# Optimization experiments

Hardware: AMD Instinct MI355X
Metric: run time of the kernel (lower is better)

## Reference

```python
import jax, jax.numpy as jnp
import numpy as np

# --- config (mirrors EV_TGN init + data attributes) ---
WIDTH, HEIGHT, TIME_WINDOW = 640, 480, 1_000_000  # data.width/height/time_window
RADIUS_NORM = 0.01                                # args.radius
MAX_NEIGHBORS = 16                                # args.max_neighbors
WINDOW = 256                                      # backward candidate window (approximates per-pixel queues, max_queue_size=128)
B, NPG = 4, 32768                                 # num_graphs, events per graph
N = B * NPG
RADIUS_PX = int(RADIUS_NORM * WIDTH + 1)          # init_graph_creator
DELTA_T = int(RADIUS_NORM * TIME_WINDOW)


def setup_inputs() -> dict:
    key = jax.random.key(0)
    kxy, kt = jax.random.split(key)
    xy = jax.random.uniform(kxy, (N, 2), dtype=jnp.float32)
    # timestamps sorted within each graph (events arrive time-ordered)
    t = jnp.sort(jax.random.uniform(kt, (B, NPG), dtype=jnp.float32), axis=1).reshape(N, 1)
    pos = jnp.concatenate([xy, t], axis=1)  # normalized (x, y, t) in [0,1]
    batch = jnp.repeat(jnp.arange(B, dtype=jnp.int32), NPG)
    return {"pos": pos, "batch": batch}


def _build_edges(pos, batch):
    # denormalize_pos: (denorm * pos + 0.001).int()
    denorm = jnp.array([WIDTH, HEIGHT, TIME_WINDOW], dtype=jnp.float32)
    p = (denorm[None, :] * pos + 0.001).astype(jnp.int32)  # [N,3] int pixel/us coords

    n = p.shape[0]
    i_idx = jnp.arange(n, dtype=jnp.int32)[:, None]       # [N,1] destination
    off = jnp.arange(1, WINDOW + 1, dtype=jnp.int32)[None, :]  # [1,W] recency offsets
    j_idx = i_idx - off                                   # [N,W] candidate sources (most recent first)
    in_range = j_idx >= 0
    j_c = jnp.clip(j_idx, 0, n - 1)

    same_b = batch[j_c] == batch[:, None]
    dxy = p[:, None, :2] - p[j_c, :2]                     # [N,W,2]
    dist2 = jnp.sum(dxy * dxy, axis=-1)
    dt = p[:, None, 2] - p[j_c, 2]
    mask = in_range & same_b & (dist2 <= RADIUS_PX * RADIUS_PX) & (dt >= 0) & (dt <= DELTA_T)

    # keep the MAX_NEIGHBORS most recent valid neighbors per destination
    rank = jnp.cumsum(mask.astype(jnp.int32), axis=1)     # 1-based recency rank
    keep = mask & (rank <= MAX_NEIGHBORS)
    slot = jnp.where(keep, rank - 1, MAX_NEIGHBORS)       # dropped entries -> dummy column
    src = jnp.full((n, MAX_NEIGHBORS + 1), -1, dtype=jnp.int32)
    rows = jnp.broadcast_to(jnp.arange(n)[:, None], slot.shape)
    src = src.at[rows, slot].set(jnp.where(keep, j_idx, -1).astype(jnp.int32))
    src = src[:, :MAX_NEIGHBORS]                          # [N,K], -1 padded
    dst = jnp.broadcast_to(jnp.arange(n, dtype=jnp.int32)[:, None], src.shape)
    dst = jnp.where(src >= 0, dst, -1)
    # edge_index: row0 = source (earlier event), row1 = destination; -1 marks padding
    return jnp.stack([src.reshape(-1), dst.reshape(-1)], axis=0)


def reference(pos, batch):
    return _build_edges(pos, batch)
```

## Files before the change

kernel.cpp:

```cpp
#include <hip/hip_runtime.h>

#define NPG    32768
#define NTOT   131072
#define MAXN   16
#define RAD2   49
#define DTMAX  10000u
#define NPB    64
#define GX     20
#define GY     16
#define NCELL  (GX*GY)
#define SLOTS  16

__global__ __launch_bounds__(256, 5)
void tgn_edges_kernel(const float* __restrict__ pos, int* __restrict__ out) {
    __shared__ int2 sp[320];
    __shared__ int  cellcnt[NCELL];
    __shared__ int  cells[NCELL][SLOTS];
    __shared__ int  fin[NPB][MAXN];

    const int tid = threadIdx.x;
    const int b0  = blockIdx.x * NPB;

    {
        const int4 m1 = make_int4(-1, -1, -1, -1);
        int4* c4 = reinterpret_cast<int4*>(&cells[0][0]);
        #pragma unroll
        for (int k = 0; k < 5; ++k) c4[k * 256 + tid] = m1;
        cellcnt[tid] = 0;
        if (tid < NCELL - 256) cellcnt[256 + tid] = 0;
        reinterpret_cast<int4*>(&fin[0][0])[tid] = m1;
    }
    __syncthreads();

    #pragma unroll
    for (int s = 0; s < 2; ++s) {
        const int idx = s * 256 + tid;
        if (s == 0 || tid < 320 - 256) {
            const int node = b0 - 256 + idx;
            if (node >= 0) {
                const float x  = pos[3 * node + 0];
                const float y  = pos[3 * node + 1];
                const float tt = pos[3 * node + 2];
                const int px = (int)(__fadd_rn(__fmul_rn(640.0f,     x),  0.001f));
                const int py = (int)(__fadd_rn(__fmul_rn(480.0f,     y),  0.001f));
                const int pt = (int)(__fadd_rn(__fmul_rn(1000000.0f, tt), 0.001f));
                sp[idx] = make_int2(px | (py << 16), pt);
                const int cell = ((py * 2185) >> 16) * GX + (px >> 5);
                const int slot = atomicAdd(&cellcnt[cell], 1);
                if (slot < SLOTS) cells[cell][slot] = idx;
            }
        }
    }
    __syncthreads();

    const int n    = tid >> 2;
    const int qq   = tid & 3;
    const int lane = tid & 63;
    const int2 pown = sp[256 + n];
    const int x  = pown.x & 0xffff;
    const int y  = pown.x >> 16;
    const int it = pown.y;

    const int xlo = x > 7 ? x - 7 : 0;
    const int xhi = x < 632 ? x + 7 : 639;
    const int ylo = y > 7 ? y - 7 : 0;
    const int yhi = y < 472 ? y + 7 : 479;
    const int cx0 = xlo >> 5,              cx1 = xhi >> 5;
    const int cy0 = (ylo * 2185) >> 16,    cy1 = (yhi * 2185) >> 16;
    const int cx  = (qq & 1) ? cx1 : cx0;
    const int cy  = (qq & 2) ? cy1 : cy0;
    const bool dup = (((qq & 1) != 0) & (cx1 == cx0)) | (((qq & 2) != 0) & (cy1 == cy0));
    const int cell = cy * GX + cx;
    int c = dup ? 0 : cellcnt[cell];
    c = c > SLOTS ? SLOTS : c;

    const int boff   = b0 & (NPG - 1);
    const int idxmin = (256 - boff) > n ? (256 - boff) : n;
    const int idxmax = n + 255;

    unsigned bm = 0;
    if (c > 0) {
        const int4 s4 = *reinterpret_cast<const int4*>(&cells[cell][0]);
        const int sl[4] = {s4.x, s4.y, s4.z, s4.w};
        #pragma unroll
        for (int k = 0; k < 4; ++k) {
            const int idx = sl[k];
            bool ok = (k < c) & (idx >= idxmin) & (idx <= idxmax);
            const int ii = ok ? idx : 0;
            const int2 pj = sp[ii];
            const int dx = x - (pj.x & 0xffff);
            const int dy = y - (pj.x >> 16);
            const unsigned dt = (unsigned)(it - pj.y);
            ok = ok & (dx * dx + dy * dy <= RAD2) & (dt <= DTMAX);
            bm |= ok ? (1u << k) : 0u;
        }
        if (c > 4) {
            for (int k = 4; k < c; ++k) {
                const int idx = cells[cell][k];
                bool ok = (idx >= idxmin) & (idx <= idxmax);
                const int ii = ok ? idx : 0;
                const int2 pj = sp[ii];
                const int dx = x - (pj.x & 0xffff);
                const int dy = y - (pj.x >> 16);
                const unsigned dt = (unsigned)(it - pj.y);
                ok = ok & (dx * dx + dy * dy <= RAD2) & (dt <= DTMAX);
                bm |= ok ? (1u << k) : 0u;
            }
        }
    }

    const int gb = lane & ~3;
    unsigned bmq[4];
    int      clq[4];
    #pragma unroll
    for (int q2 = 0; q2 < 4; ++q2) {
        bmq[q2] = __shfl(bm,   gb + q2);
        clq[q2] = __shfl(cell, gb + q2);
    }
    if (qq == 0 && (bmq[0] | bmq[1] | bmq[2] | bmq[3])) {
        int m = 0;
        #pragma unroll
        for (int q2 = 0; q2 < 4; ++q2) {
            unsigned mm = bmq[q2];
            const int cl = clq[q2];
            while (mm) {
                const int k = __ffs(mm) - 1;
                mm &= mm - 1;
                const int j = b0 - 256 + cells[cl][k];
                int p = m < MAXN ? m : MAXN;
                while (p > 0 && fin[n][p - 1] < j) {
                    if (p < MAXN) fin[n][p] = fin[n][p - 1];
                    --p;
                }
                if (p < MAXN) fin[n][p] = j;
                ++m;
            }
        }
    }
    __syncthreads();

    {
        const size_t base4 = (size_t)b0 * MAXN / 4;
        int4* __restrict__ gsrc = reinterpret_cast<int4*>(out) + base4;
        int4* __restrict__ gdst = reinterpret_cast<int4*>(out + (size_t)NTOT * MAXN) + base4;
        const int4 v = reinterpret_cast<const int4*>(&fin[0][0])[tid];
        const int row = b0 + (tid >> 2);
        int4 d;
        d.x = (v.x >= 0) ? row : -1;
        d.y = (v.y >= 0) ? row : -1;
        d.z = (v.z >= 0) ? row : -1;
        d.w = (v.w >= 0) ? row : -1;
        gsrc[tid] = v;
        gdst[tid] = d;
    }
}

extern "C" void kernel_launch(void* const* d_in, const int* in_sizes, int n_in,
                              void* d_out, int out_size, void* d_ws, size_t ws_size,
                              hipStream_t stream) {
    const float* pos = (const float*)d_in[0];
    int* out = (int*)d_out;
    tgn_edges_kernel<<<NTOT / NPB, 256, 0, stream>>>(pos, out);
}
```

Before: 13.43 us.

## Process 256 nodes per block with one thread per node over a 512-event window

Each block now handles 256 destination nodes instead of 64, with one thread per node looping over up to four grid cells. The old scheme used four threads per node plus shuffles. The shared window grows to 512 events, so the 256-event history load and cell binning are amortized over four times as many nodes and the cells-array initialization is dropped. In exchange there are fewer, heavier blocks (occupancy hint lowered to 2), serial per-thread cell loops with more divergence, and fewer blocks in total (512) to spread across the CUs.

```diff
diff --git a/kernel.cpp b/kernel.cpp
--- a/kernel.cpp
+++ b/kernel.cpp
@@ -5,15 +5,16 @@
 #define MAXN   16
 #define RAD2   49
 #define DTMAX  10000u
-#define NPB    64
+#define NPB    256
+#define WINSZ  512
 #define GX     20
 #define GY     16
 #define NCELL  (GX*GY)
 #define SLOTS  16
 
-__global__ __launch_bounds__(256, 5)
+__global__ __launch_bounds__(256, 2)
 void tgn_edges_kernel(const float* __restrict__ pos, int* __restrict__ out) {
-    __shared__ int2 sp[320];
+    __shared__ int2 sp[WINSZ];
     __shared__ int  cellcnt[NCELL];
     __shared__ int  cells[NCELL][SLOTS];
     __shared__ int  fin[NPB][MAXN];
@@ -21,41 +22,40 @@
     const int tid = threadIdx.x;
     const int b0  = blockIdx.x * NPB;
 
+    cellcnt[tid] = 0;
+    if (tid < NCELL - 256) cellcnt[256 + tid] = 0;
     {
         const int4 m1 = make_int4(-1, -1, -1, -1);
-        int4* c4 = reinterpret_cast<int4*>(&cells[0][0]);
+        int4* f4 = reinterpret_cast<int4*>(&fin[0][0]);
         #pragma unroll
-        for (int k = 0; k < 5; ++k) c4[k * 256 + tid] = m1;
-        cellcnt[tid] = 0;
-        if (tid < NCELL - 256) cellcnt[256 + tid] = 0;
-        reinterpret_cast<int4*>(&fin[0][0])[tid] = m1;
+        for (int k = 0; k < 4; ++k) f4[k * 256 + tid] = m1;
     }
     __syncthreads();
 
     #pragma unroll
     for (int s = 0; s < 2; ++s) {
-        const int idx = s * 256 + tid;
-        if (s == 0 || tid < 320 - 256) {
-            const int node = b0 - 256 + idx;
-            if (node >= 0) {
-                const float x  = pos[3 * node + 0];
-                const float y  = pos[3 * node + 1];
-                const float tt = pos[3 * node + 2];
-                const int px = (int)(__fadd_rn(__fmul_rn(640.0f,     x),  0.001f));
-                const int py = (int)(__fadd_rn(__fmul_rn(480.0f,     y),  0.001f));
-                const int pt = (int)(__fadd_rn(__fmul_rn(1000000.0f, tt), 0.001f));
-                sp[idx] = make_int2(px | (py << 16), pt);
+        const int idx  = s * 256 + tid;
+        const int node = b0 - 256 + idx;
+        int2 v = make_int2(0, 0);
+        if (node >= 0) {
+            const float x  = pos[3 * node + 0];
+            const float y  = pos[3 * node + 1];
+            const float tt = pos[3 * node + 2];
+            const int px = (int)(__fadd_rn(__fmul_rn(640.0f,     x),  0.001f));
+            const int py = (int)(__fadd_rn(__fmul_rn(480.0f,     y),  0.001f));
+            const int pt = (int)(__fadd_rn(__fmul_rn(1000000.0f, tt), 0.001f));
+            v = make_int2(px | (py << 16), pt);
+            if (idx != WINSZ - 1) {
                 const int cell = ((py * 2185) >> 16) * GX + (px >> 5);
                 const int slot = atomicAdd(&cellcnt[cell], 1);
                 if (slot < SLOTS) cells[cell][slot] = idx;
             }
         }
+        sp[idx] = v;
     }
     __syncthreads();
 
-    const int n    = tid >> 2;
-    const int qq   = tid & 3;
-    const int lane = tid & 63;
+    const int n  = tid;
     const int2 pown = sp[256 + n];
     const int x  = pown.x & 0xffff;
     const int y  = pown.x >> 16;
@@ -65,68 +65,53 @@
     const int xhi = x < 632 ? x + 7 : 639;
     const int ylo = y > 7 ? y - 7 : 0;
     const int yhi = y < 472 ? y + 7 : 479;
-    const int cx0 = xlo >> 5,              cx1 = xhi >> 5;
-    const int cy0 = (ylo * 2185) >> 16,    cy1 = (yhi * 2185) >> 16;
-    const int cx  = (qq & 1) ? cx1 : cx0;
-    const int cy  = (qq & 2) ? cy1 : cy0;
-    const bool dup = (((qq & 1) != 0) & (cx1 == cx0)) | (((qq & 2) != 0) & (cy1 == cy0));
-    const int cell = cy * GX + cx;
-    int c = dup ? 0 : cellcnt[cell];
-    c = c > SLOTS ? SLOTS : c;
+    const int cx0 = xlo >> 5,           cx1 = xhi >> 5;
+    const int cy0 = (ylo * 2185) >> 16, cy1 = (yhi * 2185) >> 16;
 
     const int boff   = b0 & (NPG - 1);
     const int idxmin = (256 - boff) > n ? (256 - boff) : n;
     const int idxmax = n + 255;
 
-    unsigned bm = 0;
-    if (c > 0) {
-        const int4 s4 = *reinterpret_cast<const int4*>(&cells[cell][0]);
-        const int sl[4] = {s4.x, s4.y, s4.z, s4.w};
-        #pragma unroll
-        for (int k = 0; k < 4; ++k) {
-            const int idx = sl[k];
-            bool ok = (k < c) & (idx >= idxmin) & (idx <= idxmax);
-            const int ii = ok ? idx : 0;
-            const int2 pj = sp[ii];
-            const int dx = x - (pj.x & 0xffff);
-            const int dy = y - (pj.x >> 16);
-            const unsigned dt = (unsigned)(it - pj.y);
-            ok = ok & (dx * dx + dy * dy <= RAD2) & (dt <= DTMAX);
-            bm |= ok ? (1u << k) : 0u;
-        }
-        if (c > 4) {
-            for (int k = 4; k < c; ++k) {
-                const int idx = cells[cell][k];
-                bool ok = (idx >= idxmin) & (idx <= idxmax);
-                const int ii = ok ? idx : 0;
-                const int2 pj = sp[ii];
-                const int dx = x - (pj.x & 0xffff);
-                const int dy = y - (pj.x >> 16);
-                const unsigned dt = (unsigned)(it - pj.y);
-                ok = ok & (dx * dx + dy * dy <= RAD2) & (dt <= DTMAX);
-                bm |= ok ? (1u << k) : 0u;
+    int m = 0;
+    for (int cy = cy0; cy <= cy1; ++cy) {
+        for (int cx = cx0; cx <= cx1; ++cx) {
+            const int cell = cy * GX + cx;
+            int c = cellcnt[cell];
+            c = c > SLOTS ? SLOTS : c;
+            unsigned bm = 0;
+            if (c > 0) {
+                const int4 s4 = *reinterpret_cast<const int4*>(&cells[cell][0]);
+                const int sl[4] = {s4.x, s4.y, s4.z, s4.w};
+                #pragma unroll
+                for (int k = 0; k < 4; ++k) {
+                    const int idx = sl[k];
+                    bool ok = (k < c) & (idx >= idxmin) & (idx <= idxmax);
+                    const int ii = ok ? idx : 0;
+                    const int2 pj = sp[ii];
+                    const int dx = x - (pj.x & 0xffff);
+                    const int dy = y - (pj.x >> 16);
+                    const unsigned dt = (unsigned)(it - pj.y);
+                    ok = ok & (dx * dx + dy * dy <= RAD2) & (dt <= DTMAX);
+                    bm |= ok ? (1u << k) : 0u;
+                }
+                if (c > 4) {
+                    for (int k = 4; k < c; ++k) {
+                        const int idx = cells[cell][k];
+                        bool ok = (idx >= idxmin) & (idx <= idxmax);
+                        const int ii = ok ? idx : 0;
+                        const int2 pj = sp[ii];
+                        const int dx = x - (pj.x & 0xffff);
+                        const int dy = y - (pj.x >> 16);
+                        const unsigned dt = (unsigned)(it - pj.y);
+                        ok = ok & (dx * dx + dy * dy <= RAD2) & (dt <= DTMAX);
+                        bm |= ok ? (1u << k) : 0u;
+                    }
+                }
             }
-        }
-    }
-
-    const int gb = lane & ~3;
-    unsigned bmq[4];
-    int      clq[4];
-    #pragma unroll
-    for (int q2 = 0; q2 < 4; ++q2) {
-        bmq[q2] = __shfl(bm,   gb + q2);
-        clq[q2] = __shfl(cell, gb + q2);
-    }
-    if (qq == 0 && (bmq[0] | bmq[1] | bmq[2] | bmq[3])) {
-        int m = 0;
-        #pragma unroll
-        for (int q2 = 0; q2 < 4; ++q2) {
-            unsigned mm = bmq[q2];
-            const int cl = clq[q2];
-            while (mm) {
-                const int k = __ffs(mm) - 1;
-                mm &= mm - 1;
-                const int j = b0 - 256 + cells[cl][k];
+            while (bm) {
+                const int k = __ffs(bm) - 1;
+                bm &= bm - 1;
+                const int j = b0 - 256 + cells[cell][k];
                 int p = m < MAXN ? m : MAXN;
                 while (p > 0 && fin[n][p - 1] < j) {
                     if (p < MAXN) fin[n][p] = fin[n][p - 1];
@@ -143,15 +128,20 @@
         const size_t base4 = (size_t)b0 * MAXN / 4;
         int4* __restrict__ gsrc = reinterpret_cast<int4*>(out) + base4;
         int4* __restrict__ gdst = reinterpret_cast<int4*>(out + (size_t)NTOT * MAXN) + base4;
-        const int4 v = reinterpret_cast<const int4*>(&fin[0][0])[tid];
-        const int row = b0 + (tid >> 2);
-        int4 d;
-        d.x = (v.x >= 0) ? row : -1;
-        d.y = (v.y >= 0) ? row : -1;
-        d.z = (v.z >= 0) ? row : -1;
-        d.w = (v.w >= 0) ? row : -1;
-        gsrc[tid] = v;
-        gdst[tid] = d;
+        const int4* f4 = reinterpret_cast<const int4*>(&fin[0][0]);
+        #pragma unroll
+        for (int k = 0; k < 4; ++k) {
+            const int flat = k * 256 + tid;
+            const int4 v = f4[flat];
+            const int row = b0 + (flat >> 2);
+            int4 d;
+            d.x = (v.x >= 0) ? row : -1;
+            d.y = (v.y >= 0) ? row : -1;
+            d.z = (v.z >= 0) ? row : -1;
+            d.w = (v.w >= 0) ? row : -1;
+            gsrc[flat] = v;
+            gdst[flat] = d;
+        }
     }
 }
 
```

Result: faster. 13.09 us (-2.5%).
